# Optimization experiments

Measured on AMD Instinct MI355X. Metric: run time of the kernel, lower is better.

The kernel has to match this reference:

```python
import jax, jax.numpy as jnp
import numpy as np

GRAPH_WEIGHT = 0.3


def setup_inputs() -> dict:
    key = jax.random.key(0)
    ks = jax.random.split(key, 6)
    B, N, NB, MAXKV, BS = 8, 1048576, 8192, 32, 128
    logits = jax.random.normal(ks[0], (B, N, 1), dtype=jnp.float32)
    targets = jax.random.bernoulli(ks[1], 0.5, (B, N)).astype(jnp.float32)
    sup_mask = jax.random.bernoulli(ks[2], 0.1, (B, N))
    ignore_mask = jax.random.bernoulli(ks[3], 0.05, (B, N))
    kv_indices = jax.random.randint(ks[4], (B, NB, MAXKV), 0, NB)
    kv_num_blocks = jax.random.randint(ks[5], (B, NB), 0, MAXKV + 1)
    return {
        "logits": logits,
        "targets": targets,
        "sup_mask": sup_mask,
        "ignore_mask": ignore_mask,
        "kv_indices": kv_indices,
        "kv_num_blocks": kv_num_blocks,
        "block_size": BS,
    }


def _loss(logits, targets, sup_mask, ignore_mask, kv_indices, kv_num_blocks, block_size):
    x = logits.squeeze(-1)                      # [B, N]
    B, N = x.shape
    nb = N // block_size
    dt = x.dtype

    # ---- supervised BCE over sup_mask (== BCEWithLogitsLoss on gathered set) ----
    per = jnp.maximum(x, 0) - x * targets + jnp.log1p(jnp.exp(-jnp.abs(x)))
    supf = sup_mask.astype(dt)
    sup_cnt = supf.sum()
    loss_sup = jnp.where(sup_cnt > 0, (per * supf).sum() / jnp.maximum(sup_cnt, 1), jnp.asarray(0, dt))

    # ---- graph smoothness (block-sparse neighbor-mean squared error) ----
    probs = jax.nn.sigmoid(x)                   # [B, N]
    uncertain = (~ignore_mask) & (~sup_mask)
    keep = (~ignore_mask).astype(dt)

    pblk = probs.reshape(B, nb, block_size)     # [B, nb, BS]
    kblk = keep.reshape(B, nb, block_size)
    block_sum = (pblk * kblk).sum(-1)           # [B, nb] sum of non-ignored probs per block
    block_cnt = kblk.sum(-1)                    # [B, nb]

    max_kv = kv_indices.shape[-1]
    flat_idx = kv_indices.reshape(B, nb * max_kv)
    g_sum = jnp.take_along_axis(block_sum, flat_idx, axis=1).reshape(B, nb, max_kv)
    g_cnt = jnp.take_along_axis(block_cnt, flat_idx, axis=1).reshape(B, nb, max_kv)
    kv_valid = (jnp.arange(max_kv)[None, None, :] < kv_num_blocks[..., None]).astype(dt)
    neigh_sum = (g_sum * kv_valid).sum(-1)      # [B, nb]
    neigh_cnt = (g_cnt * kv_valid).sum(-1)
    neigh_mean = neigh_sum / jnp.maximum(neigh_cnt, 1)

    ublk = uncertain.reshape(B, nb, block_size).astype(dt)
    q_cnt = ublk.sum(-1)                        # [B, nb] uncertain q nodes per block
    valid_block = (q_cnt > 0) & (kv_num_blocks > 0) & (neigh_cnt > 0)

    sq = (((pblk - neigh_mean[..., None]) ** 2) * ublk).sum(-1)  # [B, nb]
    vb = valid_block.astype(dt)
    loss_b = (sq * vb).sum(-1)                  # [B]
    count_b = (q_cnt * vb).sum(-1)              # [B]
    batch_valid = count_b > 0
    per_batch = jnp.where(batch_valid, loss_b / jnp.maximum(count_b, 1), 0.0)
    loss_graph = per_batch.sum() / jnp.maximum(batch_valid.sum(), 1).astype(dt)
    loss_graph = jnp.where(uncertain.any(), loss_graph, jnp.asarray(0, dt))

    return loss_sup + GRAPH_WEIGHT * loss_graph


def reference(logits, targets, sup_mask, ignore_mask, kv_indices, kv_num_blocks, block_size):
    return _loss(logits, targets, sup_mask, ignore_mask, kv_indices, kv_num_blocks, block_size)
```

## Files before the change

### kernel.cpp

```cpp
#include <hip/hip_runtime.h>

constexpr int BATCH = 8;
constexpr int NPB   = 1 << 20;
constexpr int BS    = 128;
constexpr int NB    = NPB / BS;
constexpr int NBLK  = BATCH * NB;
constexpr int MAXKV = 32;

#define GRAPH_WEIGHT 0.3f

constexpr int WS_SUP   = 0;
constexpr int WS_GRAPH = 512;
constexpr int WS_ZERO  = 2048;
constexpr int WS_BSC   = 2048;
constexpr int WS_QUP   = WS_BSC + 2 * NBLK;

__global__ __launch_bounds__(256) void k_phase1(const float4* __restrict__ lg4,
                                                const float4* __restrict__ tg4,
                                                const int4* __restrict__ sm4,
                                                const int4* __restrict__ im4,
                                                float* __restrict__ ws)
{
    const int lane = threadIdx.x & 63;
    const int wid  = (blockIdx.x << 2) + (threadIdx.x >> 6);
    const int grp  = lane >> 3;
    const int sub  = lane & 7;
    const int blk  = (wid << 3) + grp;
    const int c0   = (blk << 5) + sub;

    float4 xv[4], tv[4];
    int4   sv[4], gv[4];
#pragma unroll
    for (int j = 0; j < 4; ++j) xv[j] = lg4[c0 + (j << 3)];
#pragma unroll
    for (int j = 0; j < 4; ++j) tv[j] = tg4[c0 + (j << 3)];
#pragma unroll
    for (int j = 0; j < 4; ++j) sv[j] = sm4[c0 + (j << 3)];
#pragma unroll
    for (int j = 0; j < 4; ++j) gv[j] = im4[c0 + (j << 3)];

    float sup_sum = 0.f, sup_cnt = 0.f;
    float bsum = 0.f, bcnt = 0.f, q = 0.f, up = 0.f, up2 = 0.f;

#pragma unroll
    for (int j = 0; j < 4; ++j) {
        const float xs[4]  = {xv[j].x, xv[j].y, xv[j].z, xv[j].w};
        const float ts[4]  = {tv[j].x, tv[j].y, tv[j].z, tv[j].w};
        const int   ssv[4] = {sv[j].x, sv[j].y, sv[j].z, sv[j].w};
        const int   ggv[4] = {gv[j].x, gv[j].y, gv[j].z, gv[j].w};

#pragma unroll
        for (int k = 0; k < 4; ++k) {
            const float x = xs[k], t = ts[k];
            const bool s = (ssv[k] != 0);
            const bool g = (ggv[k] != 0);

            const float ax  = fabsf(x);
            const float e   = __expf(-ax);
            const float lp  = __logf(1.f + e);
            const float per = fmaxf(x, 0.f) - x * t + lp;
            const float inv = 1.f / (1.f + e);
            const float p   = (x >= 0.f) ? inv : e * inv;

            if (s) { sup_sum += per; sup_cnt += 1.f; }
            if (!g) { bsum += p; bcnt += 1.f; }
            if (!g && !s) { q += 1.f; up += p; up2 += p * p; }
        }
    }

#pragma unroll
    for (int d = 4; d >= 1; d >>= 1) {
        bsum += __shfl_xor(bsum, d);
        bcnt += __shfl_xor(bcnt, d);
        q    += __shfl_xor(q, d);
        up   += __shfl_xor(up, d);
        up2  += __shfl_xor(up2, d);
    }
    if (sub == 0) {
        *reinterpret_cast<float2*>(ws + WS_BSC + 2 * blk) = make_float2(bsum, bcnt);
        *reinterpret_cast<float4*>(ws + WS_QUP + 4 * blk) = make_float4(q, up, up2, 0.f);
    }

#pragma unroll
    for (int d = 32; d >= 1; d >>= 1) {
        sup_sum += __shfl_xor(sup_sum, d);
        sup_cnt += __shfl_xor(sup_cnt, d);
    }
    __shared__ float lds[4][2];
    const int w = threadIdx.x >> 6;
    if (lane == 0) { lds[w][0] = sup_sum; lds[w][1] = sup_cnt; }
    __syncthreads();
    if (threadIdx.x == 0) {
        const float a = lds[0][0] + lds[1][0] + lds[2][0] + lds[3][0];
        const float b = lds[0][1] + lds[1][1] + lds[2][1] + lds[3][1];
        float* slot = ws + WS_SUP + (int)(blockIdx.x & 63) * 8;
        atomicAdd(slot + 0, a);
        atomicAdd(slot + 1, b);
    }
}

__global__ __launch_bounds__(256) void k_phase2(const int* __restrict__ kvi,
                                                const int* __restrict__ kvn,
                                                float* __restrict__ ws)
{
    const int tid    = blockIdx.x * 256 + threadIdx.x;
    const int h      = tid >> 5;
    const int lane32 = threadIdx.x & 31;
    const int b      = h >> 13;

    const int nkv = kvn[h];
    const int idx = kvi[(size_t)h * MAXKV + lane32];

    float gs = 0.f, gc = 0.f;
    if (lane32 < nkv) {
        const int src = (h & ~(NB - 1)) + idx;
        const float2 v = *reinterpret_cast<const float2*>(ws + WS_BSC + 2 * src);
        gs = v.x; gc = v.y;
    }
#pragma unroll
    for (int d = 16; d >= 1; d >>= 1) {
        gs += __shfl_xor(gs, d);
        gc += __shfl_xor(gc, d);
    }

    __shared__ float lds[8][3];
    if (lane32 == 0) {
        const float4 quv = *reinterpret_cast<const float4*>(ws + WS_QUP + 4 * h);
        const float q = quv.x, up = quv.y, up2 = quv.z;
        const float m  = gs / fmaxf(gc, 1.f);
        const bool  vb = (q > 0.f) && (nkv > 0) && (gc > 0.f);
        const float sq = up2 - 2.f * m * up + m * m * q;
        const int hw = threadIdx.x >> 5;
        lds[hw][0] = vb ? sq : 0.f;
        lds[hw][1] = vb ? q  : 0.f;
        lds[hw][2] = q;
    }
    __syncthreads();
    if (threadIdx.x == 0) {
        float L = 0.f, C = 0.f, U = 0.f;
#pragma unroll
        for (int j = 0; j < 8; ++j) { L += lds[j][0]; C += lds[j][1]; U += lds[j][2]; }
        float* slot = ws + WS_GRAPH + b * 128 + (int)(blockIdx.x & 15) * 8;
        atomicAdd(slot + 0, L);
        atomicAdd(slot + 1, C);
        atomicAdd(slot + 2, U);
    }
}

__global__ __launch_bounds__(64) void k_phase3(const float* __restrict__ ws,
                                               float* __restrict__ out)
{
    const int lane = threadIdx.x;

    float ss = ws[WS_SUP + lane * 8 + 0];
    float sc = ws[WS_SUP + lane * 8 + 1];
#pragma unroll
    for (int d = 32; d >= 1; d >>= 1) {
        ss += __shfl_xor(ss, d);
        sc += __shfl_xor(sc, d);
    }

    float per_sum = 0.f, nvalid = 0.f, uc = 0.f;
    for (int b = 0; b < BATCH; ++b) {
        float l = 0.f, c = 0.f, u = 0.f;
        if (lane < 16) {
            l = ws[WS_GRAPH + b * 128 + lane * 8 + 0];
            c = ws[WS_GRAPH + b * 128 + lane * 8 + 1];
            u = ws[WS_GRAPH + b * 128 + lane * 8 + 2];
        }
#pragma unroll
        for (int d = 32; d >= 1; d >>= 1) {
            l += __shfl_xor(l, d);
            c += __shfl_xor(c, d);
            u += __shfl_xor(u, d);
        }
        if (c > 0.f) { per_sum += l / fmaxf(c, 1.f); nvalid += 1.f; }
        uc += u;
    }

    if (lane == 0) {
        const float loss_sup = (sc > 0.f) ? ss / fmaxf(sc, 1.f) : 0.f;
        float lg = per_sum / fmaxf(nvalid, 1.f);
        if (!(uc > 0.f)) lg = 0.f;
        out[0] = loss_sup + GRAPH_WEIGHT * lg;
    }
}

extern "C" void kernel_launch(void* const* d_in, const int* in_sizes, int n_in,
                              void* d_out, int out_size, void* d_ws, size_t ws_size,
                              hipStream_t stream) {
    const float4* lg4 = (const float4*)d_in[0];
    const float4* tg4 = (const float4*)d_in[1];
    const int4*   sm4 = (const int4*)d_in[2];
    const int4*   im4 = (const int4*)d_in[3];
    const int*    kvi = (const int*)d_in[4];
    const int*    kvn = (const int*)d_in[5];
    float* ws  = (float*)d_ws;
    float* out = (float*)d_out;

    hipMemsetAsync(d_ws, 0, WS_ZERO * sizeof(float), stream);

    k_phase1<<<(BATCH * NPB) / (16 * 256), 256, 0, stream>>>(lg4, tg4, sm4, im4, ws);
    k_phase2<<<(NBLK * 32) / 256, 256, 0, stream>>>(kvi, kvn, ws);
    k_phase3<<<1, 64, 0, stream>>>(ws, out);
}
```

Measured before the change: 196.7 us.

## Replace atomics and memset with per-workgroup partials, nontemporal loads, finer phase1 split

Phase 1 now handles 8 elements per thread, using 16 lanes per 128-element block, and launches twice as many workgroups. All streaming inputs are read with nontemporal loads, including kv_indices, which are now loaded as int4 vectors. The hipMemsetAsync and the global atomicAdd slots are gone: each workgroup writes its own partial sums, and a single 1024-thread phase-3 workgroup reduces them. This removes a launch and atomic contention, but phase 3 now has more data to reduce serially.

```diff
diff --git a/kernel.cpp b/kernel.cpp
--- a/kernel.cpp
+++ b/kernel.cpp
@@ -9,51 +9,51 @@
 
 #define GRAPH_WEIGHT 0.3f
 
-constexpr int WS_SUP   = 0;
-constexpr int WS_GRAPH = 512;
-constexpr int WS_ZERO  = 2048;
-constexpr int WS_BSC   = 2048;
-constexpr int WS_QUP   = WS_BSC + 2 * NBLK;
-
-__global__ __launch_bounds__(256) void k_phase1(const float4* __restrict__ lg4,
-                                                const float4* __restrict__ tg4,
-                                                const int4* __restrict__ sm4,
-                                                const int4* __restrict__ im4,
+constexpr int P1_WGS = (BATCH * NPB) / (256 * 8);
+constexpr int P2_WGS = NBLK / 8;
+
+constexpr int WS_BSC = 0;
+constexpr int WS_QUP = 2 * NBLK;
+constexpr int WS_SUP = WS_QUP + 4 * NBLK;
+constexpr int WS_P2  = WS_SUP + 2 * P1_WGS;
+
+typedef float v4f __attribute__((ext_vector_type(4)));
+typedef int   v4i __attribute__((ext_vector_type(4)));
+
+__global__ __launch_bounds__(256) void k_phase1(const v4f* __restrict__ lg4,
+                                                const v4f* __restrict__ tg4,
+                                                const v4i* __restrict__ sm4,
+                                                const v4i* __restrict__ im4,
                                                 float* __restrict__ ws)
 {
     const int lane = threadIdx.x & 63;
     const int wid  = (blockIdx.x << 2) + (threadIdx.x >> 6);
-    const int grp  = lane >> 3;
-    const int sub  = lane & 7;
-    const int blk  = (wid << 3) + grp;
+    const int grp  = lane >> 4;
+    const int sub  = lane & 15;
+    const int blk  = (wid << 2) + grp;
     const int c0   = (blk << 5) + sub;
 
-    float4 xv[4], tv[4];
-    int4   sv[4], gv[4];
-#pragma unroll
-    for (int j = 0; j < 4; ++j) xv[j] = lg4[c0 + (j << 3)];
-#pragma unroll
-    for (int j = 0; j < 4; ++j) tv[j] = tg4[c0 + (j << 3)];
-#pragma unroll
-    for (int j = 0; j < 4; ++j) sv[j] = sm4[c0 + (j << 3)];
-#pragma unroll
-    for (int j = 0; j < 4; ++j) gv[j] = im4[c0 + (j << 3)];
+    v4f xv[2], tv[2];
+    v4i sv[2], gv[2];
+    xv[0] = __builtin_nontemporal_load(lg4 + c0);
+    xv[1] = __builtin_nontemporal_load(lg4 + c0 + 16);
+    tv[0] = __builtin_nontemporal_load(tg4 + c0);
+    tv[1] = __builtin_nontemporal_load(tg4 + c0 + 16);
+    sv[0] = __builtin_nontemporal_load(sm4 + c0);
+    sv[1] = __builtin_nontemporal_load(sm4 + c0 + 16);
+    gv[0] = __builtin_nontemporal_load(im4 + c0);
+    gv[1] = __builtin_nontemporal_load(im4 + c0 + 16);
 
     float sup_sum = 0.f, sup_cnt = 0.f;
     float bsum = 0.f, bcnt = 0.f, q = 0.f, up = 0.f, up2 = 0.f;
 
 #pragma unroll
-    for (int j = 0; j < 4; ++j) {
-        const float xs[4]  = {xv[j].x, xv[j].y, xv[j].z, xv[j].w};
-        const float ts[4]  = {tv[j].x, tv[j].y, tv[j].z, tv[j].w};
-        const int   ssv[4] = {sv[j].x, sv[j].y, sv[j].z, sv[j].w};
-        const int   ggv[4] = {gv[j].x, gv[j].y, gv[j].z, gv[j].w};
-
+    for (int j = 0; j < 2; ++j) {
 #pragma unroll
         for (int k = 0; k < 4; ++k) {
-            const float x = xs[k], t = ts[k];
-            const bool s = (ssv[k] != 0);
-            const bool g = (ggv[k] != 0);
+            const float x = xv[j][k], t = tv[j][k];
+            const bool s = (sv[j][k] != 0);
+            const bool g = (gv[j][k] != 0);
 
             const float ax  = fabsf(x);
             const float e   = __expf(-ax);
@@ -69,7 +69,7 @@
     }
 
 #pragma unroll
-    for (int d = 4; d >= 1; d >>= 1) {
+    for (int d = 8; d >= 1; d >>= 1) {
         bsum += __shfl_xor(bsum, d);
         bcnt += __shfl_xor(bcnt, d);
         q    += __shfl_xor(q, d);
@@ -93,23 +93,21 @@
     if (threadIdx.x == 0) {
         const float a = lds[0][0] + lds[1][0] + lds[2][0] + lds[3][0];
         const float b = lds[0][1] + lds[1][1] + lds[2][1] + lds[3][1];
-        float* slot = ws + WS_SUP + (int)(blockIdx.x & 63) * 8;
-        atomicAdd(slot + 0, a);
-        atomicAdd(slot + 1, b);
-    }
-}
-
-__global__ __launch_bounds__(256) void k_phase2(const int* __restrict__ kvi,
+        *reinterpret_cast<float2*>(ws + WS_SUP + 2 * blockIdx.x) = make_float2(a, b);
+    }
+}
+
+__global__ __launch_bounds__(256) void k_phase2(const v4i* __restrict__ kvi4,
                                                 const int* __restrict__ kvn,
                                                 float* __restrict__ ws)
 {
     const int tid    = blockIdx.x * 256 + threadIdx.x;
     const int h      = tid >> 5;
     const int lane32 = threadIdx.x & 31;
-    const int b      = h >> 13;
 
     const int nkv = kvn[h];
-    const int idx = kvi[(size_t)h * MAXKV + lane32];
+    const v4i kq = __builtin_nontemporal_load(kvi4 + (h << 3) + (lane32 >> 2));
+    const int idx = kq[lane32 & 3];
 
     float gs = 0.f, gc = 0.f;
     if (lane32 < nkv) {
@@ -140,67 +138,96 @@
         float L = 0.f, C = 0.f, U = 0.f;
 #pragma unroll
         for (int j = 0; j < 8; ++j) { L += lds[j][0]; C += lds[j][1]; U += lds[j][2]; }
-        float* slot = ws + WS_GRAPH + b * 128 + (int)(blockIdx.x & 15) * 8;
-        atomicAdd(slot + 0, L);
-        atomicAdd(slot + 1, C);
-        atomicAdd(slot + 2, U);
-    }
-}
-
-__global__ __launch_bounds__(64) void k_phase3(const float* __restrict__ ws,
-                                               float* __restrict__ out)
+        *reinterpret_cast<float4*>(ws + WS_P2 + 4 * blockIdx.x) = make_float4(L, C, U, 0.f);
+    }
+}
+
+__global__ __launch_bounds__(1024) void k_phase3(const float* __restrict__ ws,
+                                                 float* __restrict__ out)
 {
-    const int lane = threadIdx.x;
-
-    float ss = ws[WS_SUP + lane * 8 + 0];
-    float sc = ws[WS_SUP + lane * 8 + 1];
-#pragma unroll
-    for (int d = 32; d >= 1; d >>= 1) {
-        ss += __shfl_xor(ss, d);
-        sc += __shfl_xor(sc, d);
-    }
-
-    float per_sum = 0.f, nvalid = 0.f, uc = 0.f;
-    for (int b = 0; b < BATCH; ++b) {
-        float l = 0.f, c = 0.f, u = 0.f;
-        if (lane < 16) {
-            l = ws[WS_GRAPH + b * 128 + lane * 8 + 0];
-            c = ws[WS_GRAPH + b * 128 + lane * 8 + 1];
-            u = ws[WS_GRAPH + b * 128 + lane * 8 + 2];
-        }
+    const int tid  = threadIdx.x;
+    const int lane = tid & 63;
+    const int w    = tid >> 6;
+
+    __shared__ float lsup[16][2];
+    __shared__ float lb[8][16][3];
+    __shared__ float lfin[8][3];
+
+    float ss = 0.f, sc = 0.f;
+#pragma unroll
+    for (int j = 0; j < 4; ++j) {
+        const float2 v = *reinterpret_cast<const float2*>(ws + WS_SUP + 2 * (tid + j * 1024));
+        ss += v.x; sc += v.y;
+    }
+#pragma unroll
+    for (int d = 32; d >= 1; d >>= 1) { ss += __shfl_xor(ss, d); sc += __shfl_xor(sc, d); }
+    if (lane == 0) { lsup[w][0] = ss; lsup[w][1] = sc; }
+
+    float L[8], C[8], U[8];
+#pragma unroll
+    for (int b = 0; b < 8; ++b) {
+        const float4 v = *reinterpret_cast<const float4*>(ws + WS_P2 + 4 * (b * 1024 + tid));
+        L[b] = v.x; C[b] = v.y; U[b] = v.z;
+    }
+#pragma unroll
+    for (int b = 0; b < 8; ++b) {
 #pragma unroll
         for (int d = 32; d >= 1; d >>= 1) {
+            L[b] += __shfl_xor(L[b], d);
+            C[b] += __shfl_xor(C[b], d);
+            U[b] += __shfl_xor(U[b], d);
+        }
+    }
+    if (lane == 0) {
+#pragma unroll
+        for (int b = 0; b < 8; ++b) { lb[b][w][0] = L[b]; lb[b][w][1] = C[b]; lb[b][w][2] = U[b]; }
+    }
+    __syncthreads();
+
+    if (tid < 128) {
+        const int b = tid >> 4, i = tid & 15;
+        float l = lb[b][i][0], c = lb[b][i][1], u = lb[b][i][2];
+#pragma unroll
+        for (int d = 8; d >= 1; d >>= 1) {
             l += __shfl_xor(l, d);
             c += __shfl_xor(c, d);
             u += __shfl_xor(u, d);
         }
-        if (c > 0.f) { per_sum += l / fmaxf(c, 1.f); nvalid += 1.f; }
-        uc += u;
-    }
-
-    if (lane == 0) {
-        const float loss_sup = (sc > 0.f) ? ss / fmaxf(sc, 1.f) : 0.f;
-        float lg = per_sum / fmaxf(nvalid, 1.f);
-        if (!(uc > 0.f)) lg = 0.f;
-        out[0] = loss_sup + GRAPH_WEIGHT * lg;
+        if (i == 0) { lfin[b][0] = l; lfin[b][1] = c; lfin[b][2] = u; }
+    }
+    __syncthreads();
+
+    if (tid == 0) {
+        float ssum = 0.f, scn = 0.f;
+#pragma unroll
+        for (int j = 0; j < 16; ++j) { ssum += lsup[j][0]; scn += lsup[j][1]; }
+        float per = 0.f, nv = 0.f, uc = 0.f;
+#pragma unroll
+        for (int b = 0; b < 8; ++b) {
+            const float l = lfin[b][0], c = lfin[b][1], u = lfin[b][2];
+            if (c > 0.f) { per += l / fmaxf(c, 1.f); nv += 1.f; }
+            uc += u;
+        }
+        const float loss_sup = (scn > 0.f) ? ssum / fmaxf(scn, 1.f) : 0.f;
+        float lgr = per / fmaxf(nv, 1.f);
+        if (!(uc > 0.f)) lgr = 0.f;
+        out[0] = loss_sup + GRAPH_WEIGHT * lgr;
     }
 }
 
 extern "C" void kernel_launch(void* const* d_in, const int* in_sizes, int n_in,
                               void* d_out, int out_size, void* d_ws, size_t ws_size,
                               hipStream_t stream) {
-    const float4* lg4 = (const float4*)d_in[0];
-    const float4* tg4 = (const float4*)d_in[1];
-    const int4*   sm4 = (const int4*)d_in[2];
-    const int4*   im4 = (const int4*)d_in[3];
-    const int*    kvi = (const int*)d_in[4];
-    const int*    kvn = (const int*)d_in[5];
+    const v4f* lg4 = (const v4f*)d_in[0];
+    const v4f* tg4 = (const v4f*)d_in[1];
+    const v4i* sm4 = (const v4i*)d_in[2];
+    const v4i* im4 = (const v4i*)d_in[3];
+    const v4i* kvi4 = (const v4i*)d_in[4];
+    const int* kvn  = (const int*)d_in[5];
     float* ws  = (float*)d_ws;
     float* out = (float*)d_out;
 
-    hipMemsetAsync(d_ws, 0, WS_ZERO * sizeof(float), stream);
-
-    k_phase1<<<(BATCH * NPB) / (16 * 256), 256, 0, stream>>>(lg4, tg4, sm4, im4, ws);
-    k_phase2<<<(NBLK * 32) / 256, 256, 0, stream>>>(kvi, kvn, ws);
-    k_phase3<<<1, 64, 0, stream>>>(ws, out);
-}
+    k_phase1<<<P1_WGS, 256, 0, stream>>>(lg4, tg4, sm4, im4, ws);
+    k_phase2<<<P2_WGS, 256, 0, stream>>>(kvi4, kvn, ws);
+    k_phase3<<<1, 1024, 0, stream>>>(ws, out);
+}
```

New measurement: 171.7 us. 1.15x faster.
